# Performance work log

Hardware: AMD Instinct MI355X
Metric: run time of the kernel (lower is better)

Reference implementation:

```python
import jax, jax.numpy as jnp
import numpy as np

PATCH = 9
EMBED = 768

def setup_inputs() -> dict:
    key = jax.random.key(0)
    k1, k2, k3, k4, k5, k6 = jax.random.split(key, 6)
    B, T, C, H, W = 4, 16, 3, 256, 256
    N = 8192
    patch_dim = PATCH * PATCH * C  # 243
    frames = jax.random.normal(k1, (B, T, C, H, W), dtype=jnp.float32)
    coords = jax.random.uniform(k2, (B, N, 2), dtype=jnp.float32)
    t_src = jax.random.randint(k3, (B, N), 0, T, dtype=jnp.int32)
    # MLP params (Linear: y = x @ W + b), kaiming-ish scale
    W1 = jax.random.normal(k4, (patch_dim, EMBED), dtype=jnp.float32) / np.sqrt(patch_dim)
    b1 = jnp.zeros((EMBED,), dtype=jnp.float32)
    W2 = jax.random.normal(k5, (EMBED, EMBED), dtype=jnp.float32) / np.sqrt(EMBED)
    b2 = jnp.zeros((EMBED,), dtype=jnp.float32)
    return {"frames": frames, "coords": coords, "t_src": t_src,
            "W1": W1, "b1": b1, "W2": W2, "b2": b2}

def reference(frames, coords, t_src, W1, b1, W2, b2):
    B, T, C, H, W = frames.shape
    N = coords.shape[1]
    half = PATCH // 2
    # integer center pixel (coords in [0,1] -> truncation == floor for nonneg)
    u = (coords[..., 0] * (W - 1)).astype(jnp.int32)  # (B, N)
    v = (coords[..., 1] * (H - 1)).astype(jnp.int32)
    off = jnp.arange(PATCH, dtype=jnp.int32) - half    # (P,)
    # replicate padding at borders == clamped gather indices
    ys = jnp.clip(v[..., None] + off, 0, H - 1)        # (B, N, P)
    xs = jnp.clip(u[..., None] + off, 0, W - 1)        # (B, N, P)
    fp = jnp.transpose(frames, (0, 1, 3, 4, 2))        # (B, T, H, W, C)
    bidx = jnp.arange(B, dtype=jnp.int32)[:, None, None, None]
    # gather patches: (B, N, P, P, C)
    patches = fp[bidx, t_src[:, :, None, None].astype(jnp.int32),
                 ys[:, :, :, None], xs[:, :, None, :]]
    x = patches.reshape(B, N, PATCH * PATCH * C)       # (B, N, 243)
    h = jax.nn.gelu(x @ W1 + b1, approximate=False)    # torch nn.GELU = exact erf
    return h @ W2 + b2                                 # (B, N, EMBED)
```

## Files before the change

### kernel.cpp

```cpp
#include <hip/hip_runtime.h>
#include <math.h>


typedef __attribute__((ext_vector_type(8))) short short8;
typedef __attribute__((ext_vector_type(4))) float floatx4;

#define M_ROWS 32768
#define KPAD   256
#define EMB    768

typedef __attribute__((address_space(1))) const void g_void;
typedef __attribute__((address_space(3))) void l_void;

__device__ __forceinline__ unsigned short f2bf(float f) {
    union { float f; unsigned int i; } w;
    w.f = f;
    unsigned int x = w.i;
    x += 0x7fffu + ((x >> 16) & 1u);
    return (unsigned short)(x >> 16);
}

__global__ void k_transpose_w1(const float* __restrict__ W1,
                               unsigned short* __restrict__ W1T) {
    int idx = blockIdx.x * 256 + threadIdx.x;
    int n  = idx >> 8;
    int kp = idx & 255;
    unsigned short v = 0;
    if (kp < 243) {
        int c = kp / 81;
        int r = kp - c * 81;
        int i = r / 9;
        int j = r - i * 9;
        int e = i * 27 + j * 3 + c;
        v = f2bf(W1[e * EMB + n]);
    }
    W1T[idx] = v;
}

__global__ void k_transpose_w2(const float* __restrict__ W2,
                               unsigned short* __restrict__ W2T) {
    __shared__ float tile[32][33];
    int tx = threadIdx.x & 31, ty = threadIdx.x >> 5;
    int k0 = blockIdx.x * 32, n0 = blockIdx.y * 32;
#pragma unroll
    for (int i = 0; i < 4; ++i)
        tile[ty + i * 8][tx] = W2[(size_t)(k0 + ty + i * 8) * EMB + n0 + tx];
    __syncthreads();
#pragma unroll
    for (int i = 0; i < 4; ++i)
        W2T[(size_t)(n0 + ty + i * 8) * EMB + k0 + tx] = f2bf(tile[tx][ty + i * 8]);
}

__global__ void k_gather(const float* __restrict__ frames,
                         const float* __restrict__ coords,
                         const int* __restrict__ t_src,
                         unsigned short* __restrict__ X) {
    int row  = blockIdx.x * 4 + (threadIdx.x >> 6);
    int lane = threadIdx.x & 63;
    int b = row >> 13;

    float cu = coords[row * 2 + 0];
    float cv = coords[row * 2 + 1];
    int u = (int)(cu * 255.0f);
    int v = (int)(cv * 255.0f);
    int t = t_src[row];

    const float* fb = frames + (size_t)(b * 16 + t) * (3 * 256 * 256);
    unsigned short* xr = X + (size_t)row * KPAD;

#pragma unroll
    for (int it = 0; it < 4; ++it) {
        int kp = lane + it * 64;
        unsigned short val = 0;
        if (kp < 243) {
            int c = kp / 81;
            int r = kp - c * 81;
            int i = r / 9;
            int j = r - i * 9;
            int y = v + i - 4; y = (y < 0) ? 0 : (y > 255 ? 255 : y);
            int x = u + j - 4; x = (x < 0) ? 0 : (x > 255 ? 255 : x);
            val = f2bf(fb[(size_t)c * 65536 + y * 256 + x]);
        }
        xr[kp] = val;
    }
}

template <int K, bool GELU, bool OUT_F32>
__global__ __launch_bounds__(256, 3)
void k_gemm(const unsigned short* __restrict__ A,
            const unsigned short* __restrict__ BT,
            const float* __restrict__ bias,
            void* __restrict__ Cv) {
    __shared__ unsigned short As[128 * 64];
    __shared__ unsigned short Bs[128 * 64];

    int tid  = threadIdx.x;
    int wave = tid >> 6;
    int lane = tid & 63;
    int wm = (wave >> 1) * 64;
    int wn = (wave & 1) * 64;
    int lm = lane & 15;
    int lq = lane >> 4;

    int m0 = blockIdx.x * 128;
    int n0 = blockIdx.y * 128;

    floatx4 acc[4][4];
#pragma unroll
    for (int i = 0; i < 4; ++i)
#pragma unroll
        for (int j = 0; j < 4; ++j)
            acc[i][j] = (floatx4){0.f, 0.f, 0.f, 0.f};

    const unsigned short* Ag = A  + (size_t)m0 * K;
    const unsigned short* Bg = BT + (size_t)n0 * K;

    int rl    = lane >> 3;
    int pslot = lane & 7;

    for (int k0 = 0; k0 < K; k0 += 64) {
#pragma unroll
        for (int i = 0; i < 4; ++i) {
            int chunk = wave * 4 + i;
            int r     = chunk * 8 + rl;
            int lslot = pslot ^ (r & 7);
            const unsigned short* ga = Ag + (size_t)r * K + k0 + (lslot << 3);
            const unsigned short* gb = Bg + (size_t)r * K + k0 + (lslot << 3);
            __builtin_amdgcn_global_load_lds((g_void*)ga, (l_void*)(As + chunk * 512), 16, 0, 0);
            __builtin_amdgcn_global_load_lds((g_void*)gb, (l_void*)(Bs + chunk * 512), 16, 0, 0);
        }
        __syncthreads();

#pragma unroll
        for (int ks = 0; ks < 2; ++ks) {
            short8 af[4], bfr[4];
#pragma unroll
            for (int mi = 0; mi < 4; ++mi) {
                int row = wm + mi * 16 + lm;
                int ps  = ((ks << 2) + lq) ^ (row & 7);
                af[mi] = *(const short8*)(As + row * 64 + (ps << 3));
            }
#pragma unroll
            for (int ni = 0; ni < 4; ++ni) {
                int row = wn + ni * 16 + lm;
                int ps  = ((ks << 2) + lq) ^ (row & 7);
                bfr[ni] = *(const short8*)(Bs + row * 64 + (ps << 3));
            }
#pragma unroll
            for (int mi = 0; mi < 4; ++mi)
#pragma unroll
                for (int ni = 0; ni < 4; ++ni)
                    acc[mi][ni] = __builtin_amdgcn_mfma_f32_16x16x32_bf16(
                        af[mi], bfr[ni], acc[mi][ni], 0, 0, 0);
        }
        __syncthreads();
    }

#pragma unroll
    for (int ni = 0; ni < 4; ++ni) {
        int col = n0 + wn + ni * 16 + lm;
        float bs = bias[col];
#pragma unroll
        for (int mi = 0; mi < 4; ++mi) {
            int rowb = m0 + wm + mi * 16 + lq * 4;
#pragma unroll
            for (int r = 0; r < 4; ++r) {
                float x = acc[mi][ni][r] + bs;
                if (GELU)
                    x = 0.5f * x * (1.0f + erff(x * 0.70710678118f));
                size_t idx = (size_t)(rowb + r) * EMB + col;
                if (OUT_F32)
                    ((float*)Cv)[idx] = x;
                else
                    ((unsigned short*)Cv)[idx] = f2bf(x);
            }
        }
    }
}

extern "C" void kernel_launch(void* const* d_in, const int* in_sizes, int n_in,
                              void* d_out, int out_size, void* d_ws, size_t ws_size,
                              hipStream_t stream) {
    const float* frames = (const float*)d_in[0];
    const float* coords = (const float*)d_in[1];
    const int*   t_src  = (const int*)d_in[2];
    const float* W1     = (const float*)d_in[3];
    const float* b1     = (const float*)d_in[4];
    const float* W2     = (const float*)d_in[5];
    const float* b2     = (const float*)d_in[6];
    float* out = (float*)d_out;

    char* ws = (char*)d_ws;
    unsigned short* X    = (unsigned short*)(ws);
    unsigned short* Hbuf = (unsigned short*)(ws + 16777216);
    unsigned short* W1T  = (unsigned short*)(ws + 16777216 + 50331648);
    unsigned short* W2T  = (unsigned short*)(ws + 16777216 + 50331648 + 393216);

    k_transpose_w1<<<768, 256, 0, stream>>>(W1, W1T);
    k_transpose_w2<<<dim3(24, 24), 256, 0, stream>>>(W2, W2T);

    k_gather<<<M_ROWS / 4, 256, 0, stream>>>(frames, coords, t_src, X);

    k_gemm<KPAD, true, false><<<dim3(M_ROWS / 128, EMB / 128), 256, 0, stream>>>(X, W1T, b1, Hbuf);

    k_gemm<EMB, false, true><<<dim3(M_ROWS / 128, EMB / 128), 256, 0, stream>>>(Hbuf, W2T, b2, out);
}
```

Measured before the change: 244.5 us.

## Double-buffer GEMM LDS tiles and bucket gather rows by frame for locality

The GEMM kernel now keeps two LDS buffers and prefetches the next K-tile with global_load_lds while computing on the current one, removing the trailing barrier. LDS use doubles, so launch bounds drop to 2 blocks per SM. Separately, rows are counting-sorted by (batch, frame) through new count/scan/scatter kernels. The gather then visits rows grouped by frame, which should improve cache reuse on frame reads. This adds four small kernel launches plus atomics, and X keeps the original row order because only the read order changes.

```diff
diff --git a/kernel.cpp b/kernel.cpp
--- a/kernel.cpp
+++ b/kernel.cpp
@@ -51,11 +51,42 @@
         W2T[(size_t)(n0 + ty + i * 8) * EMB + k0 + tx] = f2bf(tile[tx][ty + i * 8]);
 }
 
+__global__ void k_zero64(int* __restrict__ p) { p[threadIdx.x] = 0; }
+
+__global__ void k_count(const int* __restrict__ t_src, int* __restrict__ cnt) {
+    int row = blockIdx.x * 256 + threadIdx.x;
+    int bucket = (row >> 13) * 16 + t_src[row];
+    atomicAdd(&cnt[bucket], 1);
+}
+
+__global__ void k_scan64(const int* __restrict__ cnt, int* __restrict__ offs) {
+    __shared__ int s[64];
+    int i = threadIdx.x;
+    s[i] = cnt[i];
+    __syncthreads();
+    if (i == 0) {
+        int acc = 0;
+        for (int j = 0; j < 64; ++j) { int c = s[j]; s[j] = acc; acc += c; }
+    }
+    __syncthreads();
+    offs[i] = s[i];
+}
+
+__global__ void k_scatter(const int* __restrict__ t_src, int* __restrict__ offs,
+                          int* __restrict__ perm) {
+    int row = blockIdx.x * 256 + threadIdx.x;
+    int bucket = (row >> 13) * 16 + t_src[row];
+    int pos = atomicAdd(&offs[bucket], 1);
+    perm[pos] = row;
+}
+
 __global__ void k_gather(const float* __restrict__ frames,
                          const float* __restrict__ coords,
                          const int* __restrict__ t_src,
+                         const int* __restrict__ perm,
                          unsigned short* __restrict__ X) {
-    int row  = blockIdx.x * 4 + (threadIdx.x >> 6);
+    int pos  = blockIdx.x * 4 + (threadIdx.x >> 6);
+    int row  = perm[pos];
     int lane = threadIdx.x & 63;
     int b = row >> 13;
 
@@ -86,13 +117,13 @@
 }
 
 template <int K, bool GELU, bool OUT_F32>
-__global__ __launch_bounds__(256, 3)
+__global__ __launch_bounds__(256, 2)
 void k_gemm(const unsigned short* __restrict__ A,
             const unsigned short* __restrict__ BT,
             const float* __restrict__ bias,
             void* __restrict__ Cv) {
-    __shared__ unsigned short As[128 * 64];
-    __shared__ unsigned short Bs[128 * 64];
+    __shared__ unsigned short As[2][128 * 64];
+    __shared__ unsigned short Bs[2][128 * 64];
 
     int tid  = threadIdx.x;
     int wave = tid >> 6;
@@ -118,18 +149,35 @@
     int rl    = lane >> 3;
     int pslot = lane & 7;
 
+#pragma unroll
+    for (int i = 0; i < 4; ++i) {
+        int chunk = wave * 4 + i;
+        int r     = chunk * 8 + rl;
+        int lslot = pslot ^ (r & 7);
+        __builtin_amdgcn_global_load_lds((g_void*)(Ag + (size_t)r * K + (lslot << 3)),
+                                         (l_void*)(&As[0][chunk * 512]), 16, 0, 0);
+        __builtin_amdgcn_global_load_lds((g_void*)(Bg + (size_t)r * K + (lslot << 3)),
+                                         (l_void*)(&Bs[0][chunk * 512]), 16, 0, 0);
+    }
+
+    int buf = 0;
     for (int k0 = 0; k0 < K; k0 += 64) {
-#pragma unroll
-        for (int i = 0; i < 4; ++i) {
-            int chunk = wave * 4 + i;
-            int r     = chunk * 8 + rl;
-            int lslot = pslot ^ (r & 7);
-            const unsigned short* ga = Ag + (size_t)r * K + k0 + (lslot << 3);
-            const unsigned short* gb = Bg + (size_t)r * K + k0 + (lslot << 3);
-            __builtin_amdgcn_global_load_lds((g_void*)ga, (l_void*)(As + chunk * 512), 16, 0, 0);
-            __builtin_amdgcn_global_load_lds((g_void*)gb, (l_void*)(Bs + chunk * 512), 16, 0, 0);
-        }
         __syncthreads();
+
+        if (k0 + 64 < K) {
+#pragma unroll
+            for (int i = 0; i < 4; ++i) {
+                int chunk = wave * 4 + i;
+                int r     = chunk * 8 + rl;
+                int lslot = pslot ^ (r & 7);
+                __builtin_amdgcn_global_load_lds(
+                    (g_void*)(Ag + (size_t)r * K + k0 + 64 + (lslot << 3)),
+                    (l_void*)(&As[buf ^ 1][chunk * 512]), 16, 0, 0);
+                __builtin_amdgcn_global_load_lds(
+                    (g_void*)(Bg + (size_t)r * K + k0 + 64 + (lslot << 3)),
+                    (l_void*)(&Bs[buf ^ 1][chunk * 512]), 16, 0, 0);
+            }
+        }
 
 #pragma unroll
         for (int ks = 0; ks < 2; ++ks) {
@@ -138,13 +186,13 @@
             for (int mi = 0; mi < 4; ++mi) {
                 int row = wm + mi * 16 + lm;
                 int ps  = ((ks << 2) + lq) ^ (row & 7);
-                af[mi] = *(const short8*)(As + row * 64 + (ps << 3));
+                af[mi] = *(const short8*)(&As[buf][row * 64 + (ps << 3)]);
             }
 #pragma unroll
             for (int ni = 0; ni < 4; ++ni) {
                 int row = wn + ni * 16 + lm;
                 int ps  = ((ks << 2) + lq) ^ (row & 7);
-                bfr[ni] = *(const short8*)(Bs + row * 64 + (ps << 3));
+                bfr[ni] = *(const short8*)(&Bs[buf][row * 64 + (ps << 3)]);
             }
 #pragma unroll
             for (int mi = 0; mi < 4; ++mi)
@@ -153,7 +201,7 @@
                     acc[mi][ni] = __builtin_amdgcn_mfma_f32_16x16x32_bf16(
                         af[mi], bfr[ni], acc[mi][ni], 0, 0, 0);
         }
-        __syncthreads();
+        buf ^= 1;
     }
 
 #pragma unroll
@@ -195,11 +243,19 @@
     unsigned short* Hbuf = (unsigned short*)(ws + 16777216);
     unsigned short* W1T  = (unsigned short*)(ws + 16777216 + 50331648);
     unsigned short* W2T  = (unsigned short*)(ws + 16777216 + 50331648 + 393216);
+    int* cnt  = (int*)(ws + 16777216 + 50331648 + 393216 + 1179648);
+    int* offs = cnt + 64;
+    int* perm = offs + 64;
 
     k_transpose_w1<<<768, 256, 0, stream>>>(W1, W1T);
     k_transpose_w2<<<dim3(24, 24), 256, 0, stream>>>(W2, W2T);
 
-    k_gather<<<M_ROWS / 4, 256, 0, stream>>>(frames, coords, t_src, X);
+    k_zero64<<<1, 64, 0, stream>>>(cnt);
+    k_count<<<128, 256, 0, stream>>>(t_src, cnt);
+    k_scan64<<<1, 64, 0, stream>>>(cnt, offs);
+    k_scatter<<<128, 256, 0, stream>>>(t_src, offs, perm);
+
+    k_gather<<<M_ROWS / 4, 256, 0, stream>>>(frames, coords, t_src, perm, X);
 
     k_gemm<KPAD, true, false><<<dim3(M_ROWS / 128, EMB / 128), 256, 0, stream>>>(X, W1T, b1, Hbuf);
 
```

Result: slower. 335.0 us (+37.1%).
